# Optimization experiments

Measured on AMD Instinct MI355X. Metric: run time of the kernel, lower is better.

The kernel has to match this reference:

```python
import jax, jax.numpy as jnp
import numpy as np

DIM = 1024
N_HEADS = 16
B, T = 2, 2048


def setup_inputs() -> dict:
    key = jax.random.key(0)
    ks = jax.random.split(key, 9)
    D, H = DIM, N_HEADS
    return {
        "x": jax.random.normal(ks[0], (B, T, D), dtype=jnp.float32),
        "W_in": jax.random.normal(ks[1], (3 * D + H, D), dtype=jnp.float32) * (1.0 / np.sqrt(D)),
        "conv_w": jax.random.normal(ks[2], (D, 1, 4), dtype=jnp.float32) * 0.5,  # depthwise, groups=D
        "conv_b": jax.random.normal(ks[3], (D,), dtype=jnp.float32) * 0.1,
        "decay_param": jax.random.normal(ks[4], (H,), dtype=jnp.float32) * 0.5 - 3.0,
        "gn_w": jnp.ones((D,), dtype=jnp.float32),
        "gn_b": jnp.zeros((D,), dtype=jnp.float32),
        "W_out": jax.random.normal(ks[5], (D, D), dtype=jnp.float32) * (1.0 / np.sqrt(D)),
    }


def reference(x, W_in, conv_w, conv_b, decay_param, gn_w, gn_b, W_out):
    Bs, Ts, D = x.shape
    H = decay_param.shape[0]
    K = D // H
    scale = 1.0 / np.sqrt(D)

    proj = x @ W_in.T                                   # (B,T,3D+H)
    r, v, k, w = jnp.split(proj, [D, 2 * D, 3 * D], axis=-1)

    # depthwise causal-ish conv: F.pad(3 left) + Conv1d(padding=3) => left pad 6, take first T
    k_in = jnp.transpose(k, (0, 2, 1))                  # (B,D,T)
    k_out = jax.lax.conv_general_dilated(
        k_in, conv_w, window_strides=(1,), padding=[(6, 0)],
        dimension_numbers=("NCH", "OIH", "NCH"), feature_group_count=D)
    k_out = k_out[:, :, :Ts] + conv_b[None, :, None]
    k_out = jnp.transpose(k_out, (0, 2, 1))             # (B,T,D)

    v = v * jax.nn.silu(k_out)

    decay_gate = jax.nn.sigmoid(decay_param[None, None, :] + w)  # (B,T,H)
    log_decay = -8.0 * (1.0 - decay_gate) - 0.1
    ld = jnp.transpose(log_decay, (0, 2, 1))            # (B,H,T)

    v_in = jnp.transpose(v.reshape(Bs, Ts, H, K), (0, 2, 1, 3)) * scale  # (B,H,T,K)

    # parallel scan via causal decay matrix
    cs = jnp.cumsum(ld, axis=-1)                        # (B,H,T)
    idx = jnp.arange(Ts)
    mask = idx[:, None] >= idx[None, :]                 # (T,T) causal
    L = cs[..., :, None] - cs[..., None, :]             # (B,H,T,T)
    Wd = jnp.where(mask, jnp.exp(jnp.where(mask, L, 0.0)), 0.0)
    y = jnp.einsum("bhts,bhsk->bhtk", Wd, v_in)         # (B,H,T,K)

    y = jnp.transpose(y, (0, 2, 1, 3)).reshape(Bs, Ts, D)
    out = jax.nn.silu(r) * y                            # (B,T,D)

    # GroupNorm(H groups) over channels, applied on (B,D,T)
    o = jnp.transpose(out, (0, 2, 1)).reshape(Bs, H, K, Ts)
    mean = jnp.mean(o, axis=(2, 3), keepdims=True)
    var = jnp.var(o, axis=(2, 3), keepdims=True)
    o = (o - mean) * jax.lax.rsqrt(var + 1e-5)
    o = o * gn_w.reshape(1, H, K, 1) + gn_b.reshape(1, H, K, 1)
    out = jnp.transpose(o.reshape(Bs, D, Ts), (0, 2, 1))

    return out @ W_out.T
```

## Files before the change

kernel.cpp:

```cpp
#include <hip/hip_runtime.h>

#define D_   1024
#define H_   16
#define T_   2048
#define B_   2
#define BT_  (B_*T_)
#define NIN_ 3088
#define NP_  3200
#define CHUNK_ 64
#define NCH_  (T_/CHUNK_)
#define GN_INV (1.0f/131072.0f)
#define NBLK_C (BT_ * D_ / 256)

typedef unsigned short u16;
typedef __attribute__((ext_vector_type(8))) __bf16 bf16x8;
typedef __attribute__((ext_vector_type(8))) unsigned short u16x8;
typedef __attribute__((ext_vector_type(4))) float  f32x4;

struct __align__(16) F4 { float x, y, z, w; };
struct __align__(8)  U4 { u16 x, y, z, w; };

__device__ inline u16 f2bf(float f) {
  union { float f; unsigned u; } q; q.f = f;
  unsigned r = q.u + 0x7FFFu + ((q.u >> 16) & 1u);
  return (u16)(r >> 16);
}
__device__ inline float bf2f(u16 v) {
  union { unsigned u; float f; } q; q.u = ((unsigned)v) << 16; return q.f;
}

__device__ inline void gl_lds16(const void* g, void* l) {
  __builtin_amdgcn_global_load_lds(
      (const __attribute__((address_space(1))) unsigned*)g,
      (__attribute__((address_space(3))) unsigned*)l, 16, 0, 0);
}

__global__ void cvt_all(const float* __restrict__ x, const float* __restrict__ W_in,
                        const float* __restrict__ W_out,
                        u16* __restrict__ xb, u16* __restrict__ wb, u16* __restrict__ wob) {
  const int nx = BT_ * D_ / 4, nw = NP_ * D_ / 4, no = D_ * D_ / 4;
  int q = blockIdx.x * 256 + threadIdx.x;
  if (q < nx) {
    int i = q * 4;
    F4 f = *reinterpret_cast<const F4*>(x + i);
    U4 u; u.x = f2bf(f.x); u.y = f2bf(f.y); u.z = f2bf(f.z); u.w = f2bf(f.w);
    *reinterpret_cast<U4*>(xb + i) = u;
  } else if (q < nx + nw) {
    int i = (q - nx) * 4;
    int row = i >> 10;
    U4 u; u.x = 0; u.y = 0; u.z = 0; u.w = 0;
    if (row < NIN_) {
      F4 f = *reinterpret_cast<const F4*>(W_in + i);
      u.x = f2bf(f.x); u.y = f2bf(f.y); u.z = f2bf(f.z); u.w = f2bf(f.w);
    }
    *reinterpret_cast<U4*>(wb + i) = u;
  } else if (q < nx + nw + no) {
    int i = (q - nx - nw) * 4;
    F4 f = *reinterpret_cast<const F4*>(W_out + i);
    U4 u; u.x = f2bf(f.x); u.y = f2bf(f.y); u.z = f2bf(f.z); u.w = f2bf(f.w);
    *reinterpret_cast<U4*>(wob + i) = u;
  }
}

template<bool BF16OUT>
__global__ __launch_bounds__(256, 2) void gemm_bt(
    const u16* __restrict__ A, const u16* __restrict__ Bm,
    void* __restrict__ Cv, int M, int N, int K) {
  __shared__ __align__(16) u16 As[128 * 64];
  __shared__ __align__(16) u16 Bs[128 * 64];
  const int tid  = threadIdx.x;
  const int lane = tid & 63;
  const int wid  = tid >> 6;
  const int tm = blockIdx.y * 128, tn = blockIdx.x * 128;
  const int wm = (wid >> 1) * 64,  wn = (wid & 1) * 64;
  const int krow = lane & 15;
  const int ksub = (lane >> 4) * 8;
  f32x4 acc[4][4] = {};

  for (int kt = 0; kt < K; kt += 64) {
#pragma unroll
    for (int i = 0; i < 4; ++i) {
      int e = i * 2048 + tid * 8;
      int r = e >> 6;
      int c = (((tid & 7) ^ (r & 7)) << 3);
      gl_lds16(A  + (size_t)(tm + r) * K + kt + c, &As[e]);
      gl_lds16(Bm + (size_t)(tn + r) * K + kt + c, &Bs[e]);
    }
    __syncthreads();
#pragma unroll
    for (int kk = 0; kk < 64; kk += 32) {
      bf16x8 af[4], bfr[4];
#pragma unroll
      for (int i = 0; i < 4; ++i) {
        int row = wm + i * 16 + krow;
        int b = (((kk + ksub) >> 3) ^ (row & 7)) << 3;
        af[i] = *reinterpret_cast<const bf16x8*>(&As[row * 64 + b]);
      }
#pragma unroll
      for (int i = 0; i < 4; ++i) {
        int row = wn + i * 16 + krow;
        int b = (((kk + ksub) >> 3) ^ (row & 7)) << 3;
        bfr[i] = *reinterpret_cast<const bf16x8*>(&Bs[row * 64 + b]);
      }
#pragma unroll
      for (int mi = 0; mi < 4; ++mi)
#pragma unroll
        for (int ni = 0; ni < 4; ++ni)
          acc[mi][ni] = __builtin_amdgcn_mfma_f32_16x16x32_bf16(af[mi], bfr[ni], acc[mi][ni], 0, 0, 0);
    }
    __syncthreads();
  }
  const int rb = tm + wm + (lane >> 4) * 4;
  const int cb = tn + wn + (lane & 15);
#pragma unroll
  for (int mi = 0; mi < 4; ++mi)
#pragma unroll
    for (int ni = 0; ni < 4; ++ni)
#pragma unroll
      for (int j = 0; j < 4; ++j) {
        size_t off = (size_t)(rb + mi * 16 + j) * N + cb + ni * 16;
        if constexpr (BF16OUT) ((u16*)Cv)[off] = f2bf(acc[mi][ni][j]);
        else                   ((float*)Cv)[off] = acc[mi][ni][j];
      }
}

__global__ void scanA_kernel(const u16* __restrict__ proj,
                             const float* __restrict__ conv_w,
                             const float* __restrict__ conv_b,
                             const float* __restrict__ decay,
                             float* __restrict__ vv,
                             float* __restrict__ ye, float* __restrict__ Pc,
                             float* __restrict__ pfx) {
  __shared__ __align__(16) u16 lv[CHUNK_ * 64];
  __shared__ __align__(16) u16 lk[(CHUNK_ + 8) * 64];
  int bh = blockIdx.x >> 5, c = blockIdx.x & 31;
  int b = bh >> 4, h = bh & 15;
  int k = threadIdx.x;
  int d0 = h * 64;
  int t0 = c * CHUNK_;
  int rsub = k >> 3, cblk = (k & 7) * 8;
#pragma unroll
  for (int it = 0; it < 8; ++it) {
    int r = it * 8 + rsub;
    *reinterpret_cast<u16x8*>(&lv[r * 64 + cblk]) =
      *reinterpret_cast<const u16x8*>(&proj[(size_t)(b * T_ + t0 + r) * NP_ + 1024 + d0 + cblk]);
  }
#pragma unroll
  for (int it = 0; it < 9; ++it) {
    int r = it * 8 + rsub;
    int tt = t0 + r - 6;
    u16x8 kv = {0, 0, 0, 0, 0, 0, 0, 0};
    if (tt >= 0 && tt < T_)
      kv = *reinterpret_cast<const u16x8*>(&proj[(size_t)(b * T_ + tt) * NP_ + 2048 + d0 + cblk]);
    *reinterpret_cast<u16x8*>(&lk[r * 64 + cblk]) = kv;
  }
  float wv = bf2f(proj[(size_t)(b * T_ + t0 + k) * NP_ + 3072 + h]);
  float gte = 1.f / (1.f + __expf(-(decay[h] + wv)));
  float my_a = __expf(-8.f * (1.f - gte) - 0.1f);
  int d = d0 + k;
  float cw0 = conv_w[d * 4], cw1 = conv_w[d * 4 + 1],
        cw2 = conv_w[d * 4 + 2], cw3 = conv_w[d * 4 + 3];
  float cb = conv_b[d];
  __syncthreads();
  float* V = vv + ((size_t)bh * T_ + t0) * 64 + k;
  float k0 = bf2f(lk[0 * 64 + k]), k1 = bf2f(lk[1 * 64 + k]), k2 = bf2f(lk[2 * 64 + k]);
  float y = 0.f, pf = 1.f, my_pf = 1.f;
#pragma unroll
  for (int i = 0; i < CHUNK_; ++i) {
    float k3 = bf2f(lk[(i + 3) * 64 + k]);
    float v  = bf2f(lv[i * 64 + k]);
    float kc = cb;
    kc = fmaf(k0, cw0, kc); kc = fmaf(k1, cw1, kc);
    kc = fmaf(k2, cw2, kc); kc = fmaf(k3, cw3, kc);
    float sil = kc / (1.f + __expf(-kc));
    float g = v * sil * (1.f / 32.f);
    float a = __shfl(my_a, i);
    y = fmaf(a, y, g);
    V[(size_t)i * 64] = y;
    pf *= a;
    if (i == k) my_pf = pf;
    k0 = k1; k1 = k2; k2 = k3;
  }
  pfx[(size_t)bh * T_ + t0 + k] = my_pf;
  ye[(size_t)blockIdx.x * 64 + k] = y;
  Pc[(size_t)blockIdx.x * 64 + k] = pf;
}

__global__ void comb_kernel(const float* __restrict__ ye, const float* __restrict__ Pc,
                            float* __restrict__ cin) {
  int g = blockIdx.x * 256 + threadIdx.x;
  int bh = g >> 6, k = g & 63;
  float s = 0.f;
  for (int c = 0; c < NCH_; ++c) {
    size_t i = ((size_t)bh * NCH_ + c) * 64 + k;
    cin[i] = s;
    s = ye[i] + Pc[i] * s;
  }
}

__global__ void applyC_kernel(float* __restrict__ y, const u16* __restrict__ proj,
                              const float* __restrict__ pfx, const float* __restrict__ cin,
                              float* __restrict__ part) {
  int idx = blockIdx.x * 256 + threadIdx.x;
  int k  = idx & 63;
  int t  = (idx >> 6) & 2047;
  int bh = idx >> 17;
  int b = bh >> 4, h = bh & 15;
  float ci = cin[(((size_t)bh * NCH_) + (t >> 6)) * 64 + k];
  float yf = fmaf(pfx[(size_t)bh * T_ + t], ci, y[idx]);
  float r = bf2f(proj[(size_t)(b * T_ + t) * NP_ + h * 64 + k]);
  float o = yf * (r / (1.f + __expf(-r)));
  y[idx] = o;
  float s1 = o, s2 = o * o;
#pragma unroll
  for (int m = 32; m; m >>= 1) { s1 += __shfl_xor(s1, m); s2 += __shfl_xor(s2, m); }
  __shared__ float ps[8];
  int wid = threadIdx.x >> 6, lane = threadIdx.x & 63;
  if (lane == 0) { ps[wid] = s1; ps[4 + wid] = s2; }
  __syncthreads();
  if (threadIdx.x == 0) {
    part[blockIdx.x]          = ps[0] + ps[1] + ps[2] + ps[3];
    part[NBLK_C + blockIdx.x] = ps[4] + ps[5] + ps[6] + ps[7];
  }
}

__global__ void reduce_kernel(const float* __restrict__ part, float* __restrict__ sums) {
  int bh = blockIdx.x;
  int t = threadIdx.x;
  int base = bh * 512;
  float s1 = part[base + t]           + part[base + 256 + t];
  float s2 = part[NBLK_C + base + t]  + part[NBLK_C + base + 256 + t];
#pragma unroll
  for (int m = 32; m; m >>= 1) { s1 += __shfl_xor(s1, m); s2 += __shfl_xor(s2, m); }
  __shared__ float ps[8];
  int wid = t >> 6, lane = t & 63;
  if (lane == 0) { ps[wid] = s1; ps[4 + wid] = s2; }
  __syncthreads();
  if (t == 0) {
    sums[bh]      = ps[0] + ps[1] + ps[2] + ps[3];
    sums[32 + bh] = ps[4] + ps[5] + ps[6] + ps[7];
  }
}

__global__ void applyD_kernel(const float* __restrict__ o, const float* __restrict__ sums,
                              const float* __restrict__ gn_w, const float* __restrict__ gn_b,
                              u16* __restrict__ on) {
  int idx = blockIdx.x * 256 + threadIdx.x;
  int k  = idx & 63;
  int t  = (idx >> 6) & 2047;
  int bh = idx >> 17;
  int b = bh >> 4, h = bh & 15;
  float mean = sums[bh] * GN_INV;
  float var  = sums[32 + bh] * GN_INV - mean * mean;
  float inv  = rsqrtf(var + 1e-5f);
  int d = h * 64 + k;
  float val = (o[idx] - mean) * inv * gn_w[d] + gn_b[d];
  on[(size_t)(b * T_ + t) * D_ + d] = f2bf(val);
}

extern "C" void kernel_launch(void* const* d_in, const int* in_sizes, int n_in,
                              void* d_out, int out_size, void* d_ws, size_t ws_size,
                              hipStream_t stream) {
  const float* x      = (const float*)d_in[0];
  const float* W_in   = (const float*)d_in[1];
  const float* conv_w = (const float*)d_in[2];
  const float* conv_b = (const float*)d_in[3];
  const float* decay  = (const float*)d_in[4];
  const float* gn_w   = (const float*)d_in[5];
  const float* gn_b   = (const float*)d_in[6];
  const float* W_out  = (const float*)d_in[7];

  char* p = (char*)d_ws;
  auto alloc = [&](size_t bytes) { void* r = (void*)p; p += (bytes + 255) & ~(size_t)255; return r; };
  u16*  xb   = (u16*)alloc((size_t)BT_ * D_ * 2);
  u16*  wb   = (u16*)alloc((size_t)NP_ * D_ * 2);
  u16*  wob  = (u16*)alloc((size_t)D_ * D_ * 2);
  u16*  proj = (u16*)alloc((size_t)BT_ * NP_ * 2);
  float* vv   = (float*)alloc((size_t)BT_ * D_ * 4);
  float* pfx  = (float*)alloc((size_t)B_ * H_ * T_ * 4);
  float* ye   = (float*)alloc((size_t)B_ * H_ * NCH_ * 64 * 4);
  float* Pc   = (float*)alloc((size_t)B_ * H_ * NCH_ * 64 * 4);
  float* cin  = (float*)alloc((size_t)B_ * H_ * NCH_ * 64 * 4);
  float* part = (float*)alloc((size_t)2 * NBLK_C * 4);
  float* sums = (float*)alloc(64 * 4);
  u16*  on   = xb;

  if ((size_t)(p - (char*)d_ws) > ws_size) return;

  const int nq = (BT_ * D_ + NP_ * D_ + D_ * D_) / 4;
  hipLaunchKernelGGL(cvt_all, dim3((nq + 255) / 256), dim3(256), 0, stream,
                     x, W_in, W_out, xb, wb, wob);
  hipLaunchKernelGGL((gemm_bt<true>),  dim3(NP_ / 128, BT_ / 128), dim3(256), 0, stream,
                     xb, wb, (void*)proj, BT_, NP_, D_);
  hipLaunchKernelGGL(scanA_kernel,  dim3(B_ * H_ * NCH_), dim3(64),  0, stream,
                     proj, conv_w, conv_b, decay, vv, ye, Pc, pfx);
  hipLaunchKernelGGL(comb_kernel,   dim3(8),              dim3(256), 0, stream, ye, Pc, cin);
  hipLaunchKernelGGL(applyC_kernel, dim3(NBLK_C),         dim3(256), 0, stream, vv, proj, pfx, cin, part);
  hipLaunchKernelGGL(reduce_kernel, dim3(32),             dim3(256), 0, stream, part, sums);
  hipLaunchKernelGGL(applyD_kernel, dim3(BT_ * D_ / 256), dim3(256), 0, stream, vv, sums, gn_w, gn_b, on);
  hipLaunchKernelGGL((gemm_bt<false>), dim3(D_ / 128, BT_ / 128), dim3(256), 0, stream,
                     on, wob, d_out, BT_, D_, D_);
}
```

Measured before the change: 183.7 us.

## Store scan intermediates in bf16 and vectorize elementwise GroupNorm kernels by four

```diff
diff --git a/kernel.cpp b/kernel.cpp
--- a/kernel.cpp
+++ b/kernel.cpp
@@ -10,11 +10,12 @@
 #define CHUNK_ 64
 #define NCH_  (T_/CHUNK_)
 #define GN_INV (1.0f/131072.0f)
-#define NBLK_C (BT_ * D_ / 256)
+#define NBLK_C 4096
 
 typedef unsigned short u16;
 typedef __attribute__((ext_vector_type(8))) __bf16 bf16x8;
 typedef __attribute__((ext_vector_type(8))) unsigned short u16x8;
+typedef __attribute__((ext_vector_type(4))) unsigned short u16x4;
 typedef __attribute__((ext_vector_type(4))) float  f32x4;
 
 struct __align__(16) F4 { float x, y, z, w; };
@@ -128,7 +129,7 @@
                              const float* __restrict__ conv_w,
                              const float* __restrict__ conv_b,
                              const float* __restrict__ decay,
-                             float* __restrict__ vv,
+                             u16* __restrict__ vv,
                              float* __restrict__ ye, float* __restrict__ Pc,
                              float* __restrict__ pfx) {
   __shared__ __align__(16) u16 lv[CHUNK_ * 64];
@@ -162,7 +163,7 @@
         cw2 = conv_w[d * 4 + 2], cw3 = conv_w[d * 4 + 3];
   float cb = conv_b[d];
   __syncthreads();
-  float* V = vv + ((size_t)bh * T_ + t0) * 64 + k;
+  u16* V = vv + ((size_t)bh * T_ + t0) * 64 + k;
   float k0 = bf2f(lk[0 * 64 + k]), k1 = bf2f(lk[1 * 64 + k]), k2 = bf2f(lk[2 * 64 + k]);
   float y = 0.f, pf = 1.f, my_pf = 1.f;
 #pragma unroll
@@ -176,7 +177,7 @@
     float g = v * sil * (1.f / 32.f);
     float a = __shfl(my_a, i);
     y = fmaf(a, y, g);
-    V[(size_t)i * 64] = y;
+    V[(size_t)i * 64] = f2bf(y);
     pf *= a;
     if (i == k) my_pf = pf;
     k0 = k1; k1 = k2; k2 = k3;
@@ -188,30 +189,42 @@
 
 __global__ void comb_kernel(const float* __restrict__ ye, const float* __restrict__ Pc,
                             float* __restrict__ cin) {
-  int g = blockIdx.x * 256 + threadIdx.x;
-  int bh = g >> 6, k = g & 63;
-  float s = 0.f;
+  int g4 = blockIdx.x * 256 + threadIdx.x;
+  int bh = g4 >> 4, k4 = (g4 & 15) * 4;
+  f32x4 s = {0.f, 0.f, 0.f, 0.f};
   for (int c = 0; c < NCH_; ++c) {
-    size_t i = ((size_t)bh * NCH_ + c) * 64 + k;
-    cin[i] = s;
-    s = ye[i] + Pc[i] * s;
-  }
-}
-
-__global__ void applyC_kernel(float* __restrict__ y, const u16* __restrict__ proj,
+    size_t i = ((size_t)bh * NCH_ + c) * 64 + k4;
+    *reinterpret_cast<f32x4*>(&cin[i]) = s;
+    f32x4 e = *reinterpret_cast<const f32x4*>(&ye[i]);
+    f32x4 p = *reinterpret_cast<const f32x4*>(&Pc[i]);
+    s = e + p * s;
+  }
+}
+
+__global__ void applyC_kernel(const u16* __restrict__ vv, const u16* __restrict__ proj,
                               const float* __restrict__ pfx, const float* __restrict__ cin,
-                              float* __restrict__ part) {
-  int idx = blockIdx.x * 256 + threadIdx.x;
-  int k  = idx & 63;
-  int t  = (idx >> 6) & 2047;
-  int bh = idx >> 17;
+                              u16* __restrict__ ob, float* __restrict__ part) {
+  int idx4 = blockIdx.x * 256 + threadIdx.x;
+  int k4 = (idx4 & 15) * 4;
+  int t  = (idx4 >> 4) & 2047;
+  int bh = idx4 >> 15;
   int b = bh >> 4, h = bh & 15;
-  float ci = cin[(((size_t)bh * NCH_) + (t >> 6)) * 64 + k];
-  float yf = fmaf(pfx[(size_t)bh * T_ + t], ci, y[idx]);
-  float r = bf2f(proj[(size_t)(b * T_ + t) * NP_ + h * 64 + k]);
-  float o = yf * (r / (1.f + __expf(-r)));
-  y[idx] = o;
-  float s1 = o, s2 = o * o;
+  size_t ebase = ((size_t)bh * T_ + t) * 64 + k4;
+  f32x4 ci = *reinterpret_cast<const f32x4*>(&cin[(((size_t)bh * NCH_) + (t >> 6)) * 64 + k4]);
+  float px = pfx[(size_t)bh * T_ + t];
+  u16x4 yv = *reinterpret_cast<const u16x4*>(&vv[ebase]);
+  u16x4 rv = *reinterpret_cast<const u16x4*>(&proj[(size_t)(b * T_ + t) * NP_ + h * 64 + k4]);
+  u16x4 ov;
+  float s1 = 0.f, s2 = 0.f;
+#pragma unroll
+  for (int j = 0; j < 4; ++j) {
+    float yf = fmaf(px, ci[j], bf2f(yv[j]));
+    float r = bf2f(rv[j]);
+    float o = yf * (r / (1.f + __expf(-r)));
+    ov[j] = f2bf(o);
+    s1 += o; s2 += o * o;
+  }
+  *reinterpret_cast<u16x4*>(&ob[ebase]) = ov;
 #pragma unroll
   for (int m = 32; m; m >>= 1) { s1 += __shfl_xor(s1, m); s2 += __shfl_xor(s2, m); }
   __shared__ float ps[8];
@@ -227,35 +240,35 @@
 __global__ void reduce_kernel(const float* __restrict__ part, float* __restrict__ sums) {
   int bh = blockIdx.x;
   int t = threadIdx.x;
-  int base = bh * 512;
-  float s1 = part[base + t]           + part[base + 256 + t];
-  float s2 = part[NBLK_C + base + t]  + part[NBLK_C + base + 256 + t];
+  int base = bh * 128;
+  float s1 = part[base + t]           + part[base + 64 + t];
+  float s2 = part[NBLK_C + base + t]  + part[NBLK_C + base + 64 + t];
 #pragma unroll
   for (int m = 32; m; m >>= 1) { s1 += __shfl_xor(s1, m); s2 += __shfl_xor(s2, m); }
-  __shared__ float ps[8];
-  int wid = t >> 6, lane = t & 63;
-  if (lane == 0) { ps[wid] = s1; ps[4 + wid] = s2; }
-  __syncthreads();
-  if (t == 0) {
-    sums[bh]      = ps[0] + ps[1] + ps[2] + ps[3];
-    sums[32 + bh] = ps[4] + ps[5] + ps[6] + ps[7];
-  }
-}
-
-__global__ void applyD_kernel(const float* __restrict__ o, const float* __restrict__ sums,
+  if (t == 0) { sums[bh] = s1; sums[32 + bh] = s2; }
+}
+
+__global__ void applyD_kernel(const u16* __restrict__ ob, const float* __restrict__ sums,
                               const float* __restrict__ gn_w, const float* __restrict__ gn_b,
                               u16* __restrict__ on) {
-  int idx = blockIdx.x * 256 + threadIdx.x;
-  int k  = idx & 63;
-  int t  = (idx >> 6) & 2047;
-  int bh = idx >> 17;
+  int idx4 = blockIdx.x * 256 + threadIdx.x;
+  int k4 = (idx4 & 15) * 4;
+  int t  = (idx4 >> 4) & 2047;
+  int bh = idx4 >> 15;
   int b = bh >> 4, h = bh & 15;
   float mean = sums[bh] * GN_INV;
   float var  = sums[32 + bh] * GN_INV - mean * mean;
   float inv  = rsqrtf(var + 1e-5f);
-  int d = h * 64 + k;
-  float val = (o[idx] - mean) * inv * gn_w[d] + gn_b[d];
-  on[(size_t)(b * T_ + t) * D_ + d] = f2bf(val);
+  int d = h * 64 + k4;
+  u16x4 o = *reinterpret_cast<const u16x4*>(&ob[((size_t)bh * T_ + t) * 64 + k4]);
+  F4 gw = *reinterpret_cast<const F4*>(&gn_w[d]);
+  F4 gb = *reinterpret_cast<const F4*>(&gn_b[d]);
+  u16x4 r;
+  r[0] = f2bf((bf2f(o[0]) - mean) * inv * gw.x + gb.x);
+  r[1] = f2bf((bf2f(o[1]) - mean) * inv * gw.y + gb.y);
+  r[2] = f2bf((bf2f(o[2]) - mean) * inv * gw.z + gb.z);
+  r[3] = f2bf((bf2f(o[3]) - mean) * inv * gw.w + gb.w);
+  *reinterpret_cast<u16x4*>(&on[(size_t)(b * T_ + t) * D_ + d]) = r;
 }
 
 extern "C" void kernel_launch(void* const* d_in, const int* in_sizes, int n_in,
@@ -276,7 +289,8 @@
   u16*  wb   = (u16*)alloc((size_t)NP_ * D_ * 2);
   u16*  wob  = (u16*)alloc((size_t)D_ * D_ * 2);
   u16*  proj = (u16*)alloc((size_t)BT_ * NP_ * 2);
-  float* vv   = (float*)alloc((size_t)BT_ * D_ * 4);
+  u16*  vv   = (u16*)alloc((size_t)BT_ * D_ * 2);
+  u16*  ob   = (u16*)alloc((size_t)BT_ * D_ * 2);
   float* pfx  = (float*)alloc((size_t)B_ * H_ * T_ * 4);
   float* ye   = (float*)alloc((size_t)B_ * H_ * NCH_ * 64 * 4);
   float* Pc   = (float*)alloc((size_t)B_ * H_ * NCH_ * 64 * 4);
@@ -294,10 +308,10 @@
                      xb, wb, (void*)proj, BT_, NP_, D_);
   hipLaunchKernelGGL(scanA_kernel,  dim3(B_ * H_ * NCH_), dim3(64),  0, stream,
                      proj, conv_w, conv_b, decay, vv, ye, Pc, pfx);
-  hipLaunchKernelGGL(comb_kernel,   dim3(8),              dim3(256), 0, stream, ye, Pc, cin);
-  hipLaunchKernelGGL(applyC_kernel, dim3(NBLK_C),         dim3(256), 0, stream, vv, proj, pfx, cin, part);
-  hipLaunchKernelGGL(reduce_kernel, dim3(32),             dim3(256), 0, stream, part, sums);
-  hipLaunchKernelGGL(applyD_kernel, dim3(BT_ * D_ / 256), dim3(256), 0, stream, vv, sums, gn_w, gn_b, on);
+  hipLaunchKernelGGL(comb_kernel,   dim3(2),              dim3(256), 0, stream, ye, Pc, cin);
+  hipLaunchKernelGGL(applyC_kernel, dim3(NBLK_C),         dim3(256), 0, stream, vv, proj, pfx, cin, ob, part);
+  hipLaunchKernelGGL(reduce_kernel, dim3(32),             dim3(64),  0, stream, part, sums);
+  hipLaunchKernelGGL(applyD_kernel, dim3(BT_ * D_ / 1024), dim3(256), 0, stream, ob, sums, gn_w, gn_b, on);
   hipLaunchKernelGGL((gemm_bt<false>), dim3(D_ / 128, BT_ / 128), dim3(256), 0, stream,
                      on, wob, d_out, BT_, D_, D_);
 }
```

After: 176.0 us. 4.2% less time.
